# Optimization experiments

Hardware: AMD Instinct MI355X
Metric: run time of the kernel (lower is better)

The kernel has to match this reference:

```python
import jax, jax.numpy as jnp
import numpy as np

EPS = 1e-5
GROUPS = 8


def setup_inputs() -> dict:
    key = jax.random.key(0)
    ks = jax.random.split(key, 3)
    b, c, h, w = 8, 256, 64, 64
    x = jax.random.normal(ks[0], (b, c, h, w), dtype=jnp.float32)
    # 1x1 convs are just channel matmuls; store weights as [out_ch, in_ch]
    qkv_w = jax.random.normal(ks[1], (3 * c, c), dtype=jnp.float32) * (c ** -0.5)
    qkv_b = jnp.zeros((3 * c,), dtype=jnp.float32)
    out_w = jax.random.normal(ks[2], (c, c), dtype=jnp.float32) * (c ** -0.5)
    out_b = jnp.zeros((c,), dtype=jnp.float32)
    gn_w = jnp.ones((c,), dtype=jnp.float32)
    gn_b = jnp.zeros((c,), dtype=jnp.float32)
    return {"x": x, "gn_w": gn_w, "gn_b": gn_b, "qkv_w": qkv_w,
            "qkv_b": qkv_b, "out_w": out_w, "out_b": out_b}


def _group_norm(x, gn_w, gn_b):
    # x: [b, c, h, w]; normalize per (group, sample) over (c//g, h, w)
    b, c, h, w = x.shape
    xg = x.reshape(b, GROUPS, c // GROUPS, h * w)
    mean = xg.mean(axis=(2, 3), keepdims=True)
    var = xg.var(axis=(2, 3), keepdims=True)
    xn = (xg - mean) * jax.lax.rsqrt(var + EPS)
    xn = xn.reshape(b, c, h * w)
    return xn * gn_w[None, :, None] + gn_b[None, :, None]


def reference(x, gn_w, gn_b, qkv_w, qkv_b, out_w, out_b):
    b, c, h, w = x.shape
    scale = 1.0 / np.sqrt(c).astype(np.float32)  # matches channels ** -0.5
    nx = _group_norm(x, gn_w, gn_b)                       # [b, c, n]
    qkv = jnp.einsum('oc,bcn->bon', qkv_w, nx) + qkv_b[None, :, None]
    q, k, v = qkv[:, :c], qkv[:, c:2 * c], qkv[:, 2 * c:]  # each [b, c, n]
    attn = jnp.einsum('bci,bcj->bij', q, k) * scale        # [b, n, n]
    attn = jax.nn.softmax(attn, axis=-1)
    out = jnp.einsum('bij,bcj->bci', attn, v)              # [b, c, n]
    out = jnp.einsum('oc,bcn->bon', out_w, out) + out_b[None, :, None]
    return out.reshape(b, c, h, w) + x
```

## Files before the change

### kernel.cpp

```cpp
#include <hip/hip_runtime.h>
#include <math.h>


#define Bn 8
#define Cn 256
#define HWn 4096
#define Gn 8
#define CPGn 32
#define Mqkv 768
#define EPSf 1e-5f
#define QSCALEf 0.0625f
#define RTHR 8.0f

typedef short bf16x8 __attribute__((ext_vector_type(8)));
typedef float f32x4 __attribute__((ext_vector_type(4)));

__device__ __forceinline__ unsigned short f2bf(float f) {
  union { float f; unsigned u; } v; v.f = f;
  unsigned r = v.u + 0x7FFFu + ((v.u >> 16) & 1u);
  return (unsigned short)(r >> 16);
}

__device__ __forceinline__ float bf2f(unsigned short u) {
  union { unsigned u; float f; } v; v.u = ((unsigned)u) << 16;
  return v.f;
}

__device__ __forceinline__ int cvt_pk_bf16(float lo, float hi) {
  int d;
  asm("v_cvt_pk_bf16_f32 %0, %1, %2" : "=v"(d) : "v"(lo), "v"(hi));
  return d;
}

__global__ __launch_bounds__(1024)
void gn_stats_kernel(const float* __restrict__ x, const float* __restrict__ gn_w,
                     const float* __restrict__ gn_b, float* __restrict__ s_out,
                     float* __restrict__ t_out) {
  const int b = blockIdx.x / Gn, g = blockIdx.x % Gn;
  const float4* base = (const float4*)(x + ((size_t)(b * Cn + g * CPGn)) * HWn);
  const int n4 = CPGn * HWn / 4;
  float sum = 0.f, sq = 0.f;
  for (int i = threadIdx.x; i < n4; i += 1024) {
    float4 v = base[i];
    sum += (v.x + v.y) + (v.z + v.w);
    sq  += (v.x * v.x + v.y * v.y) + (v.z * v.z + v.w * v.w);
  }
  __shared__ float ss[1024], s2[1024];
  ss[threadIdx.x] = sum; s2[threadIdx.x] = sq;
  __syncthreads();
  for (int off = 512; off > 0; off >>= 1) {
    if ((int)threadIdx.x < off) {
      ss[threadIdx.x] += ss[threadIdx.x + off];
      s2[threadIdx.x] += s2[threadIdx.x + off];
    }
    __syncthreads();
  }
  if (threadIdx.x < CPGn) {
    const float inv_n = 1.f / (float)(CPGn * HWn);
    float mean = ss[0] * inv_n;
    float var  = s2[0] * inv_n - mean * mean;
    float rstd = rsqrtf(var + EPSf);
    int c = g * CPGn + (int)threadIdx.x;
    float sc = gn_w[c] * rstd;
    s_out[b * Cn + c] = sc;
    t_out[b * Cn + c] = gn_b[c] - mean * sc;
  }
}

__global__ __launch_bounds__(256)
void affine_transpose_kernel(const float* __restrict__ x, const float* __restrict__ s_aff,
                             const float* __restrict__ t_aff, unsigned short* __restrict__ nxT) {
  const int bid = blockIdx.x;
  const int b = bid & 7, r = bid >> 3;
  const int c0 = (r & 3) * 64, n0 = (r >> 2) * 64;
  const int tid = threadIdx.x;
  __shared__ unsigned int ld32[64][33];
  const float* xb = x + ((size_t)(b * Cn + c0)) * HWn + n0;
  const int cl0 = tid >> 4, nn = (tid & 15) * 4;
#pragma unroll
  for (int it = 0; it < 4; ++it) {
    int cl = cl0 + 16 * it;
    int c = c0 + cl;
    float sc = s_aff[b * Cn + c], sh = t_aff[b * Cn + c];
    float4 v = *(const float4*)(xb + (size_t)cl * HWn + nn);
    ld32[cl][(nn >> 1) + 0] = (unsigned)cvt_pk_bf16(v.x * sc + sh, v.y * sc + sh);
    ld32[cl][(nn >> 1) + 1] = (unsigned)cvt_pk_bf16(v.z * sc + sh, v.w * sc + sh);
  }
  __syncthreads();
#pragma unroll
  for (int it = 0; it < 2; ++it) {
    int chunk = tid + 256 * it;
    int n = chunk >> 3, cg = chunk & 7;
    union { unsigned short u[8]; bf16x8 v; } o;
#pragma unroll
    for (int k = 0; k < 8; ++k) {
      unsigned w32 = ld32[cg * 8 + k][n >> 1];
      o.u[k] = (unsigned short)((n & 1) ? (w32 >> 16) : (w32 & 0xffffu));
    }
    *(bf16x8*)(nxT + ((size_t)(b * HWn + n0 + n)) * Cn + c0 + cg * 8) = o.v;
  }
}

__global__ __launch_bounds__(256, 2)
void qkv_gemm_kernel(const unsigned short* __restrict__ nxT, const float* __restrict__ w,
                     const float* __restrict__ wb, unsigned short* __restrict__ Qt,
                     unsigned short* __restrict__ Kt, unsigned short* __restrict__ Vb) {
  const int bid = blockIdx.x;
  const int b = bid & 7, r = bid >> 3;
  const int n0 = (r & 63) * 64, m0 = (r >> 6) * 128;
  const int tid = threadIdx.x;
  const int wv = tid >> 6, l = tid & 63;
  const int l15 = l & 15, lq = l >> 4;
  const int ob = m0 + wv * 32;

  bf16x8 wf[2][8];
#pragma unroll
  for (int g = 0; g < 2; ++g) {
    const float* wr = w + (size_t)(ob + g * 16 + l15) * Cn + lq * 8;
#pragma unroll
    for (int kc = 0; kc < 8; ++kc) {
      float4 a = *(const float4*)(wr + kc * 32);
      float4 c4 = *(const float4*)(wr + kc * 32 + 4);
      union { int w4[4]; bf16x8 v; } u;
      u.w4[0] = cvt_pk_bf16(a.x, a.y);  u.w4[1] = cvt_pk_bf16(a.z, a.w);
      u.w4[2] = cvt_pk_bf16(c4.x, c4.y); u.w4[3] = cvt_pk_bf16(c4.z, c4.w);
      wf[g][kc] = u.v;
    }
  }

  const unsigned short* nb = nxT + (size_t)b * HWn * Cn + lq * 8;
  f32x4 acc[2][4];
#pragma unroll
  for (int g = 0; g < 2; ++g)
#pragma unroll
    for (int s = 0; s < 4; ++s) acc[g][s] = (f32x4)(0.f);

  const bool isV = (m0 >= 512);
#pragma unroll
  for (int s = 0; s < 4; ++s) {
    const unsigned short* np = nb + (size_t)(n0 + s * 16 + l15) * Cn;
#pragma unroll
    for (int kc = 0; kc < 8; ++kc) {
      bf16x8 xf = *(const bf16x8*)(np + kc * 32);
      if (!isV) {
        acc[0][s] = __builtin_amdgcn_mfma_f32_16x16x32_bf16(wf[0][kc], xf, acc[0][s], 0, 0, 0);
        acc[1][s] = __builtin_amdgcn_mfma_f32_16x16x32_bf16(wf[1][kc], xf, acc[1][s], 0, 0, 0);
      } else {
        acc[0][s] = __builtin_amdgcn_mfma_f32_16x16x32_bf16(xf, wf[0][kc], acc[0][s], 0, 0, 0);
        acc[1][s] = __builtin_amdgcn_mfma_f32_16x16x32_bf16(xf, wf[1][kc], acc[1][s], 0, 0, 0);
      }
    }
  }

  if (!isV) {
    unsigned short* dst = (m0 < 256) ? Qt : Kt;
    const float scl = (m0 < 256) ? QSCALEf : 1.0f;
#pragma unroll
    for (int g = 0; g < 2; ++g) {
      int cb = ((ob + g * 16) & 255) + lq * 4;
      float b0 = wb[ob + g * 16 + lq * 4 + 0];
      float b1 = wb[ob + g * 16 + lq * 4 + 1];
      float b2 = wb[ob + g * 16 + lq * 4 + 2];
      float b3 = wb[ob + g * 16 + lq * 4 + 3];
#pragma unroll
      for (int s = 0; s < 4; ++s) {
        int n = n0 + s * 16 + l15;
        ushort4 pk;
        pk.x = f2bf((acc[g][s][0] + b0) * scl);
        pk.y = f2bf((acc[g][s][1] + b1) * scl);
        pk.z = f2bf((acc[g][s][2] + b2) * scl);
        pk.w = f2bf((acc[g][s][3] + b3) * scl);
        *(ushort4*)(dst + ((size_t)(b * HWn + n)) * Cn + cb) = pk;
      }
    }
  } else {
#pragma unroll
    for (int g = 0; g < 2; ++g) {
      int o = ob + g * 16 + l15;
      int c = o - 512;
      float bias = wb[o];
#pragma unroll
      for (int s = 0; s < 4; ++s) {
        int n = n0 + s * 16 + lq * 4;
        ushort4 pk;
        pk.x = f2bf(acc[g][s][0] + bias);
        pk.y = f2bf(acc[g][s][1] + bias);
        pk.z = f2bf(acc[g][s][2] + bias);
        pk.w = f2bf(acc[g][s][3] + bias);
        *(ushort4*)(Vb + ((size_t)(b * Cn + c)) * HWn + n) = pk;
      }
    }
  }
}

__global__ __launch_bounds__(256, 2)
void attn_kernel(const unsigned short* __restrict__ Qt,
                 const unsigned short* __restrict__ Kt,
                 const unsigned short* __restrict__ Vb,
                 unsigned short* __restrict__ pO, float* __restrict__ pML) {
  const int bid = blockIdx.x;
  const int b = bid & 7, part = (bid >> 3) & 3, i0 = (bid >> 5) * 64;
  const int tid = threadIdx.x;
  const int wv = tid >> 6, l = tid & 63;
  const int l15 = l & 15, lq = l >> 4;

  __shared__ unsigned short Ks[8192];
  __shared__ unsigned short Vs[8192];
  char* KsB = (char*)Ks;
  char* VsB = (char*)Vs;

  const unsigned short* Qb = Qt + ((size_t)b * HWn + i0) * Cn;
  const unsigned short* Kb = Kt + (size_t)b * HWn * Cn;
  const unsigned short* Vg = Vb + (size_t)b * Cn * HWn;

  bf16x8 qf[8];
  {
    const unsigned short* qrow = Qb + (size_t)(wv * 16 + l15) * Cn + lq * 8;
#pragma unroll
    for (int kc = 0; kc < 8; ++kc) qf[kc] = *(const bf16x8*)(qrow + kc * 32);
  }

  const int jk = ((tid >> 6) & 1) * 16 + (tid & 15);
  const int ck = (tid >> 7) * 32 + ((tid >> 4) & 3) * 8;
  const int cv = (tid >> 6) * 16 + (tid & 15);
  const int jv = ((tid >> 4) & 3) * 8;
  const unsigned short* gK = Kb + (size_t)(jk + part * 1024) * Cn + ck;
  const unsigned short* gV = Vg + (size_t)cv * HWn + jv + part * 1024;

  const int laneA = l15 + ((lq & 1) << 5);
  const int laneB = laneA + 16;
  const int shi = lq >> 1;

  bf16x8 kst[4], vst[4];
#pragma unroll
  for (int q = 0; q < 4; ++q) kst[q] = *(const bf16x8*)(gK + q * 64);
#pragma unroll
  for (int q = 0; q < 4; ++q) vst[q] = *(const bf16x8*)(gV + (size_t)q * 64 * HWn);
  gK += 32 * Cn; gV += 32;

  f32x4 o_acc[16];
#pragma unroll
  for (int cs = 0; cs < 16; ++cs) o_acc[cs] = (f32x4)(0.f);
  float m_i = -INFINITY, l_i = 0.f;

#pragma unroll 1
  for (int t = 0; t < 32; ++t) {
#pragma unroll
    for (int q = 0; q < 4; ++q) *(bf16x8*)(KsB + tid * 16 + q * 4096) = kst[q];
#pragma unroll
    for (int q = 0; q < 4; ++q) *(bf16x8*)(VsB + tid * 16 + q * 4096) = vst[q];
    __syncthreads();
    if (t < 31) {
#pragma unroll
      for (int q = 0; q < 4; ++q) kst[q] = *(const bf16x8*)(gK + q * 64);
#pragma unroll
      for (int q = 0; q < 4; ++q) vst[q] = *(const bf16x8*)(gV + (size_t)q * 64 * HWn);
      gK += 32 * Cn; gV += 32;
    }

    f32x4 s0 = (f32x4)(0.f), s1 = (f32x4)(0.f);
#pragma unroll
    for (int kc = 0; kc < 8; ++kc) {
      bf16x8 kf0 = *(const bf16x8*)(KsB + l * 16 + kc * 2048);
      bf16x8 kf1 = *(const bf16x8*)(KsB + l * 16 + kc * 2048 + 1024);
      s0 = __builtin_amdgcn_mfma_f32_16x16x32_bf16(kf0, qf[kc], s0, 0, 0, 0);
      s1 = __builtin_amdgcn_mfma_f32_16x16x32_bf16(kf1, qf[kc], s1, 0, 0, 0);
    }

    float p[2][4];
#pragma unroll
    for (int u = 0; u < 4; ++u) { p[0][u] = s0[u]; p[1][u] = s1[u]; }
    float rm = fmaxf(fmaxf(fmaxf(p[0][0], p[0][1]), fmaxf(p[0][2], p[0][3])),
                     fmaxf(fmaxf(p[1][0], p[1][1]), fmaxf(p[1][2], p[1][3])));
    rm = fmaxf(rm, __shfl_xor(rm, 16));
    rm = fmaxf(rm, __shfl_xor(rm, 32));
    if (!__all(rm - m_i <= RTHR)) {
      float mn = fmaxf(m_i, rm);
      float alpha = __expf(m_i - mn);
      m_i = mn;
      l_i *= alpha;
      float a0 = __shfl(alpha, 4 * lq + 0);
      float a1 = __shfl(alpha, 4 * lq + 1);
      float a2 = __shfl(alpha, 4 * lq + 2);
      float a3 = __shfl(alpha, 4 * lq + 3);
#pragma unroll
      for (int cs = 0; cs < 16; ++cs) {
        o_acc[cs][0] *= a0; o_acc[cs][1] *= a1;
        o_acc[cs][2] *= a2; o_acc[cs][3] *= a3;
      }
    }
    float rs = 0.f;
#pragma unroll
    for (int s = 0; s < 2; ++s)
#pragma unroll
      for (int u = 0; u < 4; ++u) { float e = __expf(p[s][u] - m_i); p[s][u] = e; rs += e; }
    rs += __shfl_xor(rs, 16);
    rs += __shfl_xor(rs, 32);
    l_i += rs;

    int d00 = cvt_pk_bf16(p[0][0], p[0][1]), d01 = cvt_pk_bf16(p[0][2], p[0][3]);
    int d10 = cvt_pk_bf16(p[1][0], p[1][1]), d11 = cvt_pk_bf16(p[1][2], p[1][3]);
    int A00 = __shfl(d00, laneA), A01 = __shfl(d01, laneA);
    int A10 = __shfl(d10, laneA), A11 = __shfl(d11, laneA);
    int B00 = __shfl(d00, laneB), B01 = __shfl(d01, laneB);
    int B10 = __shfl(d10, laneB), B11 = __shfl(d11, laneB);
    union { int w[4]; bf16x8 v; } pa;
    pa.w[0] = shi ? A10 : A00; pa.w[1] = shi ? A11 : A01;
    pa.w[2] = shi ? B10 : B00; pa.w[3] = shi ? B11 : B01;

#pragma unroll
    for (int cs = 0; cs < 16; ++cs) {
      bf16x8 vf = *(const bf16x8*)(VsB + l * 16 + cs * 1024);
      o_acc[cs] = __builtin_amdgcn_mfma_f32_16x16x32_bf16(pa.v, vf, o_acc[cs], 0, 0, 0);
    }
    __syncthreads();
  }

  unsigned short* pOb = pO + (size_t)bid * (64 * 256);
  const int ibase = wv * 16 + lq * 4;
#pragma unroll
  for (int cs = 0; cs < 16; ++cs) {
    int c = cs * 16 + l15;
    pOb[(ibase + 0) * 256 + c] = f2bf(o_acc[cs][0]);
    pOb[(ibase + 1) * 256 + c] = f2bf(o_acc[cs][1]);
    pOb[(ibase + 2) * 256 + c] = f2bf(o_acc[cs][2]);
    pOb[(ibase + 3) * 256 + c] = f2bf(o_acc[cs][3]);
  }
  if (lq == 0) {
    pML[(size_t)bid * 128 + (wv * 16 + l15) * 2 + 0] = m_i;
    pML[(size_t)bid * 128 + (wv * 16 + l15) * 2 + 1] = l_i;
  }
}

__global__ __launch_bounds__(256)
void attn_combine_kernel(unsigned short* __restrict__ pO, const float* __restrict__ pML) {
  const int bid = blockIdx.x;
  const int b = bid & 7, itile = bid >> 3;
  const int tid = threadIdx.x;
  const int p0id = b + (itile << 5);
  unsigned short* B0 = pO + (size_t)p0id * (64 * 256);
  const unsigned short* B1 = pO + (size_t)(p0id + 8)  * (64 * 256);
  const unsigned short* B2 = pO + (size_t)(p0id + 16) * (64 * 256);
  const unsigned short* B3 = pO + (size_t)(p0id + 24) * (64 * 256);

  __shared__ float gS[4][64];
  if (tid < 64) {
    float m0v = pML[(size_t)p0id * 128 + tid * 2],        l0v = pML[(size_t)p0id * 128 + tid * 2 + 1];
    float m1v = pML[(size_t)(p0id + 8) * 128 + tid * 2],  l1v = pML[(size_t)(p0id + 8) * 128 + tid * 2 + 1];
    float m2v = pML[(size_t)(p0id + 16) * 128 + tid * 2], l2v = pML[(size_t)(p0id + 16) * 128 + tid * 2 + 1];
    float m3v = pML[(size_t)(p0id + 24) * 128 + tid * 2], l3v = pML[(size_t)(p0id + 24) * 128 + tid * 2 + 1];
    float ms = fmaxf(fmaxf(m0v, m1v), fmaxf(m2v, m3v));
    float w0 = __expf(m0v - ms), w1 = __expf(m1v - ms);
    float w2 = __expf(m2v - ms), w3 = __expf(m3v - ms);
    float den = w0 * l0v + w1 * l1v + w2 * l2v + w3 * l3v;
    float id = 1.f / den;
    gS[0][tid] = w0 * id; gS[1][tid] = w1 * id;
    gS[2][tid] = w2 * id; gS[3][tid] = w3 * id;
  }
  __syncthreads();

#pragma unroll
  for (int k = 0; k < 8; ++k) {
    int chunk = tid + 256 * k;
    int row = chunk >> 5, cc = (chunk & 31) * 8;
    int off = row * 256 + cc;
    float g0 = gS[0][row], g1 = gS[1][row], g2 = gS[2][row], g3 = gS[3][row];
    union { unsigned short u[8]; bf16x8 v; } v0, v1, v2, v3, o;
    v0.v = *(const bf16x8*)(B0 + off);
    v1.v = *(const bf16x8*)(B1 + off);
    v2.v = *(const bf16x8*)(B2 + off);
    v3.v = *(const bf16x8*)(B3 + off);
#pragma unroll
    for (int e = 0; e < 8; ++e) {
      float val = g0 * bf2f(v0.u[e]) + g1 * bf2f(v1.u[e]) +
                  g2 * bf2f(v2.u[e]) + g3 * bf2f(v3.u[e]);
      o.u[e] = f2bf(val);
    }
    *(bf16x8*)(B0 + off) = o.v;
  }
}

__global__ __launch_bounds__(256, 2)
void out_gemm_kernel(const unsigned short* __restrict__ pO, const float* __restrict__ w,
                     const float* __restrict__ wb, const float* __restrict__ xres,
                     float* __restrict__ y) {
  const int bid = blockIdx.x;
  const int b = bid & 7, r = bid >> 3;
  const int n0 = (r & 63) * 64, m0 = (r >> 6) * 128;
  const int tid = threadIdx.x;
  const int wv = tid >> 6, l = tid & 63;
  const int l15 = l & 15, lq = l >> 4;
  const int ob = m0 + wv * 32;

  bf16x8 wf[2][8];
#pragma unroll
  for (int g = 0; g < 2; ++g) {
    const float* wr = w + (size_t)(ob + g * 16 + l15) * Cn + lq * 8;
#pragma unroll
    for (int kc = 0; kc < 8; ++kc) {
      float4 a = *(const float4*)(wr + kc * 32);
      float4 c4 = *(const float4*)(wr + kc * 32 + 4);
      union { int w4[4]; bf16x8 v; } u;
      u.w4[0] = cvt_pk_bf16(a.x, a.y);  u.w4[1] = cvt_pk_bf16(a.z, a.w);
      u.w4[2] = cvt_pk_bf16(c4.x, c4.y); u.w4[3] = cvt_pk_bf16(c4.z, c4.w);
      wf[g][kc] = u.v;
    }
  }

  const unsigned short* tb = pO + ((size_t)(b + ((n0 >> 6) << 5)) * (64 * 256)) + lq * 8;
  f32x4 acc[2][4];
#pragma unroll
  for (int g = 0; g < 2; ++g)
#pragma unroll
    for (int s = 0; s < 4; ++s) acc[g][s] = (f32x4)(0.f);

#pragma unroll
  for (int s = 0; s < 4; ++s) {
    const unsigned short* tp = tb + (size_t)(s * 16 + l15) * Cn;
#pragma unroll
    for (int kc = 0; kc < 8; ++kc) {
      bf16x8 tf = *(const bf16x8*)(tp + kc * 32);
      acc[0][s] = __builtin_amdgcn_mfma_f32_16x16x32_bf16(tf, wf[0][kc], acc[0][s], 0, 0, 0);
      acc[1][s] = __builtin_amdgcn_mfma_f32_16x16x32_bf16(tf, wf[1][kc], acc[1][s], 0, 0, 0);
    }
  }

#pragma unroll
  for (int g = 0; g < 2; ++g) {
    int o = ob + g * 16 + l15;
    float bias = wb[o];
#pragma unroll
    for (int s = 0; s < 4; ++s) {
      int n = n0 + s * 16 + lq * 4;
      size_t idx = ((size_t)(b * Cn + o)) * HWn + n;
      float4 xr = *(const float4*)(xres + idx);
      float4 out;
      out.x = acc[g][s][0] + bias + xr.x;
      out.y = acc[g][s][1] + bias + xr.y;
      out.z = acc[g][s][2] + bias + xr.z;
      out.w = acc[g][s][3] + bias + xr.w;
      *(float4*)(y + idx) = out;
    }
  }
}

extern "C" void kernel_launch(void* const* d_in, const int* in_sizes, int n_in,
                              void* d_out, int out_size, void* d_ws, size_t ws_size,
                              hipStream_t stream) {
  (void)in_sizes; (void)n_in; (void)out_size; (void)ws_size;
  const float* x     = (const float*)d_in[0];
  const float* gn_w  = (const float*)d_in[1];
  const float* gn_b  = (const float*)d_in[2];
  const float* qkv_w = (const float*)d_in[3];
  const float* qkv_b = (const float*)d_in[4];
  const float* out_w = (const float*)d_in[5];
  const float* out_b = (const float*)d_in[6];
  float* out = (float*)d_out;

  char* ws = (char*)d_ws;
  const size_t BHC = (size_t)Bn * HWn * Cn;
  float* s_aff = (float*)ws;
  float* t_aff = s_aff + Bn * Cn;
  unsigned short* Qt  = (unsigned short*)(ws + 16384);
  unsigned short* Kt  = Qt + BHC;
  unsigned short* Vb  = Kt + BHC;
  unsigned short* nxT = Vb + BHC;
  unsigned short* pO  = nxT;
  float* pML = (float*)((char*)pO + (size_t)2048 * 16384 * 2);

  gn_stats_kernel<<<dim3(Bn * Gn), 1024, 0, stream>>>(x, gn_w, gn_b, s_aff, t_aff);
  affine_transpose_kernel<<<dim3(2048), 256, 0, stream>>>(x, s_aff, t_aff, nxT);
  qkv_gemm_kernel<<<dim3(3072), 256, 0, stream>>>(nxT, qkv_w, qkv_b, Qt, Kt, Vb);
  attn_kernel<<<dim3(2048), 256, 0, stream>>>(Qt, Kt, Vb, pO, pML);
  attn_combine_kernel<<<dim3(512), 256, 0, stream>>>(pO, pML);
  out_gemm_kernel<<<dim3(1024), 256, 0, stream>>>(pO, out_w, out_b, x, out);
}
```

Baseline: 424.5 us.

## Process two query tiles per warp and halve the KV split count

The attention kernel now gives each block 128 query rows (32 per wave, as two 16-row sets) so every K/V tile staged in shared memory feeds twice as many MFMAs. The KV split drops from four parts to two, so each block walks 2048 keys instead of 1024 and launches 512 blocks instead of 2048. The combine kernel and the out-GEMM indexing are updated to match the new partial-output layout. This lowers K/V global and LDS traffic per query and shrinks the combine work. The costs are double the accumulator registers, which may reduce occupancy or cause spills, and fewer blocks, which may underfill the 256 CUs.

New measurement: 547.9 us. 29.1% more time.

```diff
diff --git a/kernel.cpp b/kernel.cpp
--- a/kernel.cpp
+++ b/kernel.cpp
@@ -199,7 +199,7 @@
                  const unsigned short* __restrict__ Vb,
                  unsigned short* __restrict__ pO, float* __restrict__ pML) {
   const int bid = blockIdx.x;
-  const int b = bid & 7, part = (bid >> 3) & 3, i0 = (bid >> 5) * 64;
+  const int b = bid & 7, part = (bid >> 3) & 1, i0 = (bid >> 4) * 128;
   const int tid = threadIdx.x;
   const int wv = tid >> 6, l = tid & 63;
   const int l15 = l & 15, lq = l >> 4;
@@ -213,19 +213,23 @@
   const unsigned short* Kb = Kt + (size_t)b * HWn * Cn;
   const unsigned short* Vg = Vb + (size_t)b * Cn * HWn;
 
-  bf16x8 qf[8];
+  bf16x8 qfA[8], qfB[8];
   {
-    const unsigned short* qrow = Qb + (size_t)(wv * 16 + l15) * Cn + lq * 8;
-#pragma unroll
-    for (int kc = 0; kc < 8; ++kc) qf[kc] = *(const bf16x8*)(qrow + kc * 32);
+    const unsigned short* qr0 = Qb + (size_t)(wv * 32 + l15) * Cn + lq * 8;
+    const unsigned short* qr1 = qr0 + 16 * Cn;
+#pragma unroll
+    for (int kc = 0; kc < 8; ++kc) {
+      qfA[kc] = *(const bf16x8*)(qr0 + kc * 32);
+      qfB[kc] = *(const bf16x8*)(qr1 + kc * 32);
+    }
   }
 
   const int jk = ((tid >> 6) & 1) * 16 + (tid & 15);
   const int ck = (tid >> 7) * 32 + ((tid >> 4) & 3) * 8;
   const int cv = (tid >> 6) * 16 + (tid & 15);
   const int jv = ((tid >> 4) & 3) * 8;
-  const unsigned short* gK = Kb + (size_t)(jk + part * 1024) * Cn + ck;
-  const unsigned short* gV = Vg + (size_t)cv * HWn + jv + part * 1024;
+  const unsigned short* gK = Kb + (size_t)(jk + part * 2048) * Cn + ck;
+  const unsigned short* gV = Vg + (size_t)cv * HWn + jv + part * 2048;
 
   const int laneA = l15 + ((lq & 1) << 5);
   const int laneB = laneA + 16;
@@ -238,19 +242,19 @@
   for (int q = 0; q < 4; ++q) vst[q] = *(const bf16x8*)(gV + (size_t)q * 64 * HWn);
   gK += 32 * Cn; gV += 32;
 
-  f32x4 o_acc[16];
-#pragma unroll
-  for (int cs = 0; cs < 16; ++cs) o_acc[cs] = (f32x4)(0.f);
-  float m_i = -INFINITY, l_i = 0.f;
+  f32x4 oA[16], oB[16];
+#pragma unroll
+  for (int cs = 0; cs < 16; ++cs) { oA[cs] = (f32x4)(0.f); oB[cs] = (f32x4)(0.f); }
+  float mA = -INFINITY, lA = 0.f, mB = -INFINITY, lB = 0.f;
 
 #pragma unroll 1
-  for (int t = 0; t < 32; ++t) {
+  for (int t = 0; t < 64; ++t) {
 #pragma unroll
     for (int q = 0; q < 4; ++q) *(bf16x8*)(KsB + tid * 16 + q * 4096) = kst[q];
 #pragma unroll
     for (int q = 0; q < 4; ++q) *(bf16x8*)(VsB + tid * 16 + q * 4096) = vst[q];
     __syncthreads();
-    if (t < 31) {
+    if (t < 63) {
 #pragma unroll
       for (int q = 0; q < 4; ++q) kst[q] = *(const bf16x8*)(gK + q * 64);
 #pragma unroll
@@ -258,77 +262,126 @@
       gK += 32 * Cn; gV += 32;
     }
 
-    f32x4 s0 = (f32x4)(0.f), s1 = (f32x4)(0.f);
+    f32x4 sA0 = (f32x4)(0.f), sA1 = (f32x4)(0.f);
+    f32x4 sB0 = (f32x4)(0.f), sB1 = (f32x4)(0.f);
 #pragma unroll
     for (int kc = 0; kc < 8; ++kc) {
       bf16x8 kf0 = *(const bf16x8*)(KsB + l * 16 + kc * 2048);
       bf16x8 kf1 = *(const bf16x8*)(KsB + l * 16 + kc * 2048 + 1024);
-      s0 = __builtin_amdgcn_mfma_f32_16x16x32_bf16(kf0, qf[kc], s0, 0, 0, 0);
-      s1 = __builtin_amdgcn_mfma_f32_16x16x32_bf16(kf1, qf[kc], s1, 0, 0, 0);
-    }
-
-    float p[2][4];
-#pragma unroll
-    for (int u = 0; u < 4; ++u) { p[0][u] = s0[u]; p[1][u] = s1[u]; }
-    float rm = fmaxf(fmaxf(fmaxf(p[0][0], p[0][1]), fmaxf(p[0][2], p[0][3])),
-                     fmaxf(fmaxf(p[1][0], p[1][1]), fmaxf(p[1][2], p[1][3])));
-    rm = fmaxf(rm, __shfl_xor(rm, 16));
-    rm = fmaxf(rm, __shfl_xor(rm, 32));
-    if (!__all(rm - m_i <= RTHR)) {
-      float mn = fmaxf(m_i, rm);
-      float alpha = __expf(m_i - mn);
-      m_i = mn;
-      l_i *= alpha;
-      float a0 = __shfl(alpha, 4 * lq + 0);
-      float a1 = __shfl(alpha, 4 * lq + 1);
-      float a2 = __shfl(alpha, 4 * lq + 2);
-      float a3 = __shfl(alpha, 4 * lq + 3);
+      sA0 = __builtin_amdgcn_mfma_f32_16x16x32_bf16(kf0, qfA[kc], sA0, 0, 0, 0);
+      sA1 = __builtin_amdgcn_mfma_f32_16x16x32_bf16(kf1, qfA[kc], sA1, 0, 0, 0);
+      sB0 = __builtin_amdgcn_mfma_f32_16x16x32_bf16(kf0, qfB[kc], sB0, 0, 0, 0);
+      sB1 = __builtin_amdgcn_mfma_f32_16x16x32_bf16(kf1, qfB[kc], sB1, 0, 0, 0);
+    }
+
+    {
+      float p0[4], p1[4];
+#pragma unroll
+      for (int u = 0; u < 4; ++u) { p0[u] = sA0[u]; p1[u] = sA1[u]; }
+      float rm = fmaxf(fmaxf(fmaxf(p0[0], p0[1]), fmaxf(p0[2], p0[3])),
+                       fmaxf(fmaxf(p1[0], p1[1]), fmaxf(p1[2], p1[3])));
+      rm = fmaxf(rm, __shfl_xor(rm, 16));
+      rm = fmaxf(rm, __shfl_xor(rm, 32));
+      if (!__all(rm - mA <= RTHR)) {
+        float mn = fmaxf(mA, rm);
+        float alpha = __expf(mA - mn);
+        mA = mn; lA *= alpha;
+        float a0 = __shfl(alpha, 4 * lq + 0);
+        float a1 = __shfl(alpha, 4 * lq + 1);
+        float a2 = __shfl(alpha, 4 * lq + 2);
+        float a3 = __shfl(alpha, 4 * lq + 3);
+#pragma unroll
+        for (int cs = 0; cs < 16; ++cs) {
+          oA[cs][0] *= a0; oA[cs][1] *= a1; oA[cs][2] *= a2; oA[cs][3] *= a3;
+        }
+      }
+      float rs = 0.f;
+#pragma unroll
+      for (int u = 0; u < 4; ++u) { p0[u] = __expf(p0[u] - mA); rs += p0[u]; }
+#pragma unroll
+      for (int u = 0; u < 4; ++u) { p1[u] = __expf(p1[u] - mA); rs += p1[u]; }
+      rs += __shfl_xor(rs, 16);
+      rs += __shfl_xor(rs, 32);
+      lA += rs;
+
+      int d00 = cvt_pk_bf16(p0[0], p0[1]), d01 = cvt_pk_bf16(p0[2], p0[3]);
+      int d10 = cvt_pk_bf16(p1[0], p1[1]), d11 = cvt_pk_bf16(p1[2], p1[3]);
+      int A00 = __shfl(d00, laneA), A01 = __shfl(d01, laneA);
+      int A10 = __shfl(d10, laneA), A11 = __shfl(d11, laneA);
+      int B00 = __shfl(d00, laneB), B01 = __shfl(d01, laneB);
+      int B10 = __shfl(d10, laneB), B11 = __shfl(d11, laneB);
+      union { int w[4]; bf16x8 v; } pa;
+      pa.w[0] = shi ? A10 : A00; pa.w[1] = shi ? A11 : A01;
+      pa.w[2] = shi ? B10 : B00; pa.w[3] = shi ? B11 : B01;
+      float q0[4], q1[4];
+#pragma unroll
+      for (int u = 0; u < 4; ++u) { q0[u] = sB0[u]; q1[u] = sB1[u]; }
+      float rmb = fmaxf(fmaxf(fmaxf(q0[0], q0[1]), fmaxf(q0[2], q0[3])),
+                        fmaxf(fmaxf(q1[0], q1[1]), fmaxf(q1[2], q1[3])));
+      rmb = fmaxf(rmb, __shfl_xor(rmb, 16));
+      rmb = fmaxf(rmb, __shfl_xor(rmb, 32));
+      if (!__all(rmb - mB <= RTHR)) {
+        float mn = fmaxf(mB, rmb);
+        float alpha = __expf(mB - mn);
+        mB = mn; lB *= alpha;
+        float a0 = __shfl(alpha, 4 * lq + 0);
+        float a1 = __shfl(alpha, 4 * lq + 1);
+        float a2 = __shfl(alpha, 4 * lq + 2);
+        float a3 = __shfl(alpha, 4 * lq + 3);
+#pragma unroll
+        for (int cs = 0; cs < 16; ++cs) {
+          oB[cs][0] *= a0; oB[cs][1] *= a1; oB[cs][2] *= a2; oB[cs][3] *= a3;
+        }
+      }
+      float rsb = 0.f;
+#pragma unroll
+      for (int u = 0; u < 4; ++u) { q0[u] = __expf(q0[u] - mB); rsb += q0[u]; }
+#pragma unroll
+      for (int u = 0; u < 4; ++u) { q1[u] = __expf(q1[u] - mB); rsb += q1[u]; }
+      rsb += __shfl_xor(rsb, 16);
+      rsb += __shfl_xor(rsb, 32);
+      lB += rsb;
+
+      int e00 = cvt_pk_bf16(q0[0], q0[1]), e01 = cvt_pk_bf16(q0[2], q0[3]);
+      int e10 = cvt_pk_bf16(q1[0], q1[1]), e11 = cvt_pk_bf16(q1[2], q1[3]);
+      int C00 = __shfl(e00, laneA), C01 = __shfl(e01, laneA);
+      int C10 = __shfl(e10, laneA), C11 = __shfl(e11, laneA);
+      int D00 = __shfl(e00, laneB), D01 = __shfl(e01, laneB);
+      int D10 = __shfl(e10, laneB), D11 = __shfl(e11, laneB);
+      union { int w[4]; bf16x8 v; } pb;
+      pb.w[0] = shi ? C10 : C00; pb.w[1] = shi ? C11 : C01;
+      pb.w[2] = shi ? D10 : D00; pb.w[3] = shi ? D11 : D01;
+
 #pragma unroll
       for (int cs = 0; cs < 16; ++cs) {
-        o_acc[cs][0] *= a0; o_acc[cs][1] *= a1;
-        o_acc[cs][2] *= a2; o_acc[cs][3] *= a3;
+        bf16x8 vf = *(const bf16x8*)(VsB + l * 16 + cs * 1024);
+        oA[cs] = __builtin_amdgcn_mfma_f32_16x16x32_bf16(pa.v, vf, oA[cs], 0, 0, 0);
+        oB[cs] = __builtin_amdgcn_mfma_f32_16x16x32_bf16(pb.v, vf, oB[cs], 0, 0, 0);
       }
     }
-    float rs = 0.f;
-#pragma unroll
-    for (int s = 0; s < 2; ++s)
-#pragma unroll
-      for (int u = 0; u < 4; ++u) { float e = __expf(p[s][u] - m_i); p[s][u] = e; rs += e; }
-    rs += __shfl_xor(rs, 16);
-    rs += __shfl_xor(rs, 32);
-    l_i += rs;
-
-    int d00 = cvt_pk_bf16(p[0][0], p[0][1]), d01 = cvt_pk_bf16(p[0][2], p[0][3]);
-    int d10 = cvt_pk_bf16(p[1][0], p[1][1]), d11 = cvt_pk_bf16(p[1][2], p[1][3]);
-    int A00 = __shfl(d00, laneA), A01 = __shfl(d01, laneA);
-    int A10 = __shfl(d10, laneA), A11 = __shfl(d11, laneA);
-    int B00 = __shfl(d00, laneB), B01 = __shfl(d01, laneB);
-    int B10 = __shfl(d10, laneB), B11 = __shfl(d11, laneB);
-    union { int w[4]; bf16x8 v; } pa;
-    pa.w[0] = shi ? A10 : A00; pa.w[1] = shi ? A11 : A01;
-    pa.w[2] = shi ? B10 : B00; pa.w[3] = shi ? B11 : B01;
-
-#pragma unroll
-    for (int cs = 0; cs < 16; ++cs) {
-      bf16x8 vf = *(const bf16x8*)(VsB + l * 16 + cs * 1024);
-      o_acc[cs] = __builtin_amdgcn_mfma_f32_16x16x32_bf16(pa.v, vf, o_acc[cs], 0, 0, 0);
-    }
     __syncthreads();
   }
 
-  unsigned short* pOb = pO + (size_t)bid * (64 * 256);
-  const int ibase = wv * 16 + lq * 4;
+  unsigned short* pOb = pO + (size_t)bid * (128 * 256);
+  const int rA = wv * 32 + lq * 4;
+  const int rB = rA + 16;
 #pragma unroll
   for (int cs = 0; cs < 16; ++cs) {
     int c = cs * 16 + l15;
-    pOb[(ibase + 0) * 256 + c] = f2bf(o_acc[cs][0]);
-    pOb[(ibase + 1) * 256 + c] = f2bf(o_acc[cs][1]);
-    pOb[(ibase + 2) * 256 + c] = f2bf(o_acc[cs][2]);
-    pOb[(ibase + 3) * 256 + c] = f2bf(o_acc[cs][3]);
+    pOb[(rA + 0) * 256 + c] = f2bf(oA[cs][0]);
+    pOb[(rA + 1) * 256 + c] = f2bf(oA[cs][1]);
+    pOb[(rA + 2) * 256 + c] = f2bf(oA[cs][2]);
+    pOb[(rA + 3) * 256 + c] = f2bf(oA[cs][3]);
+    pOb[(rB + 0) * 256 + c] = f2bf(oB[cs][0]);
+    pOb[(rB + 1) * 256 + c] = f2bf(oB[cs][1]);
+    pOb[(rB + 2) * 256 + c] = f2bf(oB[cs][2]);
+    pOb[(rB + 3) * 256 + c] = f2bf(oB[cs][3]);
   }
   if (lq == 0) {
-    pML[(size_t)bid * 128 + (wv * 16 + l15) * 2 + 0] = m_i;
-    pML[(size_t)bid * 128 + (wv * 16 + l15) * 2 + 1] = l_i;
+    pML[(size_t)bid * 256 + (wv * 32 + l15) * 2 + 0] = mA;
+    pML[(size_t)bid * 256 + (wv * 32 + l15) * 2 + 1] = lA;
+    pML[(size_t)bid * 256 + (wv * 32 + 16 + l15) * 2 + 0] = mB;
+    pML[(size_t)bid * 256 + (wv * 32 + 16 + l15) * 2 + 1] = lB;
   }
 }
 
@@ -337,45 +390,33 @@
   const int bid = blockIdx.x;
   const int b = bid & 7, itile = bid >> 3;
   const int tid = threadIdx.x;
-  const int p0id = b + (itile << 5);
-  unsigned short* B0 = pO + (size_t)p0id * (64 * 256);
-  const unsigned short* B1 = pO + (size_t)(p0id + 8)  * (64 * 256);
-  const unsigned short* B2 = pO + (size_t)(p0id + 16) * (64 * 256);
-  const unsigned short* B3 = pO + (size_t)(p0id + 24) * (64 * 256);
-
-  __shared__ float gS[4][64];
-  if (tid < 64) {
-    float m0v = pML[(size_t)p0id * 128 + tid * 2],        l0v = pML[(size_t)p0id * 128 + tid * 2 + 1];
-    float m1v = pML[(size_t)(p0id + 8) * 128 + tid * 2],  l1v = pML[(size_t)(p0id + 8) * 128 + tid * 2 + 1];
-    float m2v = pML[(size_t)(p0id + 16) * 128 + tid * 2], l2v = pML[(size_t)(p0id + 16) * 128 + tid * 2 + 1];
-    float m3v = pML[(size_t)(p0id + 24) * 128 + tid * 2], l3v = pML[(size_t)(p0id + 24) * 128 + tid * 2 + 1];
-    float ms = fmaxf(fmaxf(m0v, m1v), fmaxf(m2v, m3v));
-    float w0 = __expf(m0v - ms), w1 = __expf(m1v - ms);
-    float w2 = __expf(m2v - ms), w3 = __expf(m3v - ms);
-    float den = w0 * l0v + w1 * l1v + w2 * l2v + w3 * l3v;
-    float id = 1.f / den;
-    gS[0][tid] = w0 * id; gS[1][tid] = w1 * id;
-    gS[2][tid] = w2 * id; gS[3][tid] = w3 * id;
+  const int p0 = b + itile * 16, p1 = p0 + 8;
+  unsigned short* B0 = pO + (size_t)p0 * (128 * 256);
+  const unsigned short* B1 = pO + (size_t)p1 * (128 * 256);
+
+  __shared__ float g0S[128], g1S[128];
+  if (tid < 128) {
+    float m0 = pML[(size_t)p0 * 256 + tid * 2], l0 = pML[(size_t)p0 * 256 + tid * 2 + 1];
+    float m1 = pML[(size_t)p1 * 256 + tid * 2], l1 = pML[(size_t)p1 * 256 + tid * 2 + 1];
+    float ms = fmaxf(m0, m1);
+    float w0 = __expf(m0 - ms), w1 = __expf(m1 - ms);
+    float id = 1.f / (w0 * l0 + w1 * l1);
+    g0S[tid] = w0 * id; g1S[tid] = w1 * id;
   }
   __syncthreads();
 
 #pragma unroll
-  for (int k = 0; k < 8; ++k) {
+  for (int k = 0; k < 16; ++k) {
     int chunk = tid + 256 * k;
     int row = chunk >> 5, cc = (chunk & 31) * 8;
     int off = row * 256 + cc;
-    float g0 = gS[0][row], g1 = gS[1][row], g2 = gS[2][row], g3 = gS[3][row];
-    union { unsigned short u[8]; bf16x8 v; } v0, v1, v2, v3, o;
+    float g0 = g0S[row], g1 = g1S[row];
+    union { unsigned short u[8]; bf16x8 v; } v0, v1, o;
     v0.v = *(const bf16x8*)(B0 + off);
     v1.v = *(const bf16x8*)(B1 + off);
-    v2.v = *(const bf16x8*)(B2 + off);
-    v3.v = *(const bf16x8*)(B3 + off);
-#pragma unroll
-    for (int e = 0; e < 8; ++e) {
-      float val = g0 * bf2f(v0.u[e]) + g1 * bf2f(v1.u[e]) +
-                  g2 * bf2f(v2.u[e]) + g3 * bf2f(v3.u[e]);
-      o.u[e] = f2bf(val);
-    }
+#pragma unroll
+    for (int e = 0; e < 8; ++e)
+      o.u[e] = f2bf(g0 * bf2f(v0.u[e]) + g1 * bf2f(v1.u[e]));
     *(bf16x8*)(B0 + off) = o.v;
   }
 }
@@ -407,7 +448,8 @@
     }
   }
 
-  const unsigned short* tb = pO + ((size_t)(b + ((n0 >> 6) << 5)) * (64 * 256)) + lq * 8;
+  const int slot = b + ((n0 >> 7) << 4);
+  const unsigned short* tb = pO + (size_t)slot * (128 * 256) + (size_t)(n0 & 127) * 256 + lq * 8;
   f32x4 acc[2][4];
 #pragma unroll
   for (int g = 0; g < 2; ++g)
@@ -416,7 +458,7 @@
 
 #pragma unroll
   for (int s = 0; s < 4; ++s) {
-    const unsigned short* tp = tb + (size_t)(s * 16 + l15) * Cn;
+    const unsigned short* tp = tb + (size_t)(s * 16 + l15) * 256;
 #pragma unroll
     for (int kc = 0; kc < 8; ++kc) {
       bf16x8 tf = *(const bf16x8*)(tp + kc * 32);
@@ -466,12 +508,12 @@
   unsigned short* Vb  = Kt + BHC;
   unsigned short* nxT = Vb + BHC;
   unsigned short* pO  = nxT;
-  float* pML = (float*)((char*)pO + (size_t)2048 * 16384 * 2);
+  float* pML = (float*)((char*)pO + (size_t)512 * 32768 * 2);
 
   gn_stats_kernel<<<dim3(Bn * Gn), 1024, 0, stream>>>(x, gn_w, gn_b, s_aff, t_aff);
   affine_transpose_kernel<<<dim3(2048), 256, 0, stream>>>(x, s_aff, t_aff, nxT);
   qkv_gemm_kernel<<<dim3(3072), 256, 0, stream>>>(nxT, qkv_w, qkv_b, Qt, Kt, Vb);
-  attn_kernel<<<dim3(2048), 256, 0, stream>>>(Qt, Kt, Vb, pO, pML);
-  attn_combine_kernel<<<dim3(512), 256, 0, stream>>>(pO, pML);
+  attn_kernel<<<dim3(512), 256, 0, stream>>>(Qt, Kt, Vb, pO, pML);
+  attn_combine_kernel<<<dim3(256), 256, 0, stream>>>(pO, pML);
   out_gemm_kernel<<<dim3(1024), 256, 0, stream>>>(pO, out_w, out_b, x, out);
 }
```
